# Kernel tuning notes

Hardware: AMD Instinct MI355X
Metric: run time of the kernel (lower is better)

Reference implementation:

```python
import jax, jax.numpy as jnp
import numpy as np
import math

B, S, D, H = 2, 1024, 4096, 32
HD = D // H  # 128
THETA = 500000.0


def setup_inputs() -> dict:
    key = jax.random.key(0)
    ks = jax.random.split(key, 6)
    x = jax.random.normal(ks[0], (B, S, D), dtype=jnp.float32)
    # RoPE frequencies (complex freqs_cis split into cos/sin), [S, HD//2]
    inv_freq = 1.0 / (THETA ** (jnp.arange(0, HD, 2, dtype=jnp.float32) / HD))
    angles = jnp.arange(S, dtype=jnp.float32)[:, None] * inv_freq[None, :]
    freqs_cos = jnp.cos(angles)
    freqs_sin = jnp.sin(angles)
    # Causal mask [1,1,S,S]: 0 on/below diag, large negative above
    neg = jnp.full((S, S), -1e9, dtype=jnp.float32)
    mask = jnp.triu(neg, k=1)[None, None]
    cache_k = jnp.zeros((B, S, H, HD), dtype=jnp.float32)
    cache_v = jnp.zeros((B, S, H, HD), dtype=jnp.float32)
    sc = 0.02
    wq = jax.random.normal(ks[1], (D, D), dtype=jnp.float32) * sc
    wk = jax.random.normal(ks[2], (D, D), dtype=jnp.float32) * sc
    wv = jax.random.normal(ks[3], (D, D), dtype=jnp.float32) * sc
    wo = jax.random.normal(ks[4], (D, D), dtype=jnp.float32) * sc
    return {"x": x, "freqs_cos": freqs_cos, "freqs_sin": freqs_sin,
            "mask": mask, "cache_k": cache_k, "cache_v": cache_v,
            "wq": wq, "wk": wk, "wv": wv, "wo": wo, "start_pos": 0}


def _apply_rope(t, cos, sin):
    # t: [B,S,H,HD]; cos/sin: [S,HD//2] -> complex multiply on (even, odd) pairs
    b, s, h, hd = t.shape
    tr = t.reshape(b, s, h, hd // 2, 2)
    te, to = tr[..., 0], tr[..., 1]
    c = cos[None, :, None, :]
    sn = sin[None, :, None, :]
    oe = te * c - to * sn
    oo = te * sn + to * c
    return jnp.stack([oe, oo], axis=-1).reshape(b, s, h, hd)


def reference(x, freqs_cos, freqs_sin, mask, cache_k, cache_v, wq, wk, wv, wo, start_pos):
    bsz, seqlen, dim = x.shape
    xq = (x @ wq.T).reshape(bsz, seqlen, H, HD)
    xk = (x @ wk.T).reshape(bsz, seqlen, H, HD)
    xv = (x @ wv.T).reshape(bsz, seqlen, H, HD)
    xq = _apply_rope(xq, freqs_cos, freqs_sin)
    xk = _apply_rope(xk, freqs_cos, freqs_sin)
    # KV-cache update
    cache_k = jax.lax.dynamic_update_slice(cache_k, xk, (0, start_pos, 0, 0))
    cache_v = jax.lax.dynamic_update_slice(cache_v, xv, (0, start_pos, 0, 0))
    keys = cache_k[:bsz, : start_pos + seqlen]    # [B,K,H,HD]
    values = cache_v[:bsz, : start_pos + seqlen]
    scores = jnp.einsum("bqhd,bkhd->bhqk", xq, keys) / math.sqrt(HD)
    scores = scores + mask
    probs = jax.nn.softmax(scores.astype(jnp.float32), axis=-1).astype(xq.dtype)
    out = jnp.einsum("bhqk,bkhd->bqhd", probs, values).reshape(bsz, seqlen, dim)
    return out @ wo.T
```

## Files before the change

### kernel.cpp

```cpp
#include <hip/hip_runtime.h>
#include <cstdint>
#include <cstddef>

typedef __bf16 bf16;
typedef bf16  bf16x8  __attribute__((ext_vector_type(8)));
typedef bf16  bf16x4  __attribute__((ext_vector_type(4)));
typedef float floatx4 __attribute__((ext_vector_type(4)));

#define D_MODEL 4096
#define NROWS   2048
#define SEQ     1024
#define NHEADS  32
#define HDIM    128

__device__ __forceinline__ void async16(const void* g, void* s) {
    __builtin_amdgcn_global_load_lds(
        (__attribute__((address_space(1))) void*)g,
        (__attribute__((address_space(3))) void*)s,
        16, 0, 0);
}

__global__ __launch_bounds__(256) void cvt_kernel(const float* __restrict__ in,
                                                  bf16* __restrict__ out, int n4) {
    int i = blockIdx.x * 256 + threadIdx.x;
    if (i >= n4) return;
    const float4 v = ((const float4*)in)[i];
    bf16x4 o;
    o[0] = (bf16)v.x; o[1] = (bf16)v.y; o[2] = (bf16)v.z; o[3] = (bf16)v.w;
    ((bf16x4*)out)[i] = o;
}

__global__ __launch_bounds__(256) void rope_kernel(bf16* __restrict__ Qb,
                                                   bf16* __restrict__ Kb,
                                                   const float* __restrict__ fc,
                                                   const float* __restrict__ fs) {
    int t = blockIdx.x * 256 + threadIdx.x;
    const bool isK = (t >> 20) != 0;
    bf16* p = isK ? Kb : Qb;
    const float qs = isK ? 1.0f : 0.08838834764831845f;
    int i = t & 1048575;
    int e = i * 8;
    int row = e >> 12;
    int coff = e & 4095;
    int s = row & 1023;
    int d0 = (coff & 127) >> 1;

    bf16x8 v = *(bf16x8*)(p + (size_t)row * D_MODEL + coff);
    float4 c4 = *(const float4*)&fc[s * 64 + d0];
    float4 s4 = *(const float4*)&fs[s * 64 + d0];
    float cc[4] = {c4.x, c4.y, c4.z, c4.w};
    float ss[4] = {s4.x, s4.y, s4.z, s4.w};
    bf16x8 o;
#pragma unroll
    for (int j = 0; j < 4; j++) {
        float e0 = (float)v[2 * j], e1 = (float)v[2 * j + 1];
        o[2 * j]     = (bf16)((e0 * cc[j] - e1 * ss[j]) * qs);
        o[2 * j + 1] = (bf16)((e0 * ss[j] + e1 * cc[j]) * qs);
    }
    *(bf16x8*)(p + (size_t)row * D_MODEL + coff) = o;
}

template<bool F32OUT>
__global__ __launch_bounds__(256) void gemm_bt(const bf16* __restrict__ A,
                                               const bf16* __restrict__ B0,
                                               void* __restrict__ C0) {
    __shared__ __align__(16) bf16 As[128 * 32];
    __shared__ __align__(16) bf16 Bs[128 * 32];
    const int tid  = threadIdx.x;
    const int lane = tid & 63;
    const int wave = tid >> 6;
    const int col  = lane & 15;
    const int quad = lane >> 4;
    const int bm = blockIdx.x * 128;
    const int bn = blockIdx.y * 128;
    const int wm = (wave >> 1) * 64;
    const int wn = (wave & 1) * 64;
    const bf16* Bw = B0 + (size_t)blockIdx.z * ((size_t)D_MODEL * D_MODEL);

    floatx4 acc[4][4] = {};

    for (int k0 = 0; k0 < D_MODEL; k0 += 32) {
#pragma unroll
        for (int j = 0; j < 2; j++) {
            int c   = j * 256 + tid;
            int row = c >> 2;
            int kc  = (c & 3) * 8;
            void* dstA = (void*)(As + (size_t)(j * 256 + wave * 64) * 8);
            void* dstB = (void*)(Bs + (size_t)(j * 256 + wave * 64) * 8);
            async16(A  + (size_t)(bm + row) * D_MODEL + k0 + kc, dstA);
            async16(Bw + (size_t)(bn + row) * D_MODEL + k0 + kc, dstB);
        }
        __syncthreads();
        bf16x8 a[4], b[4];
#pragma unroll
        for (int i = 0; i < 4; i++)
            a[i] = *(const bf16x8*)&As[(wm + i * 16 + col) * 32 + quad * 8];
#pragma unroll
        for (int j = 0; j < 4; j++)
            b[j] = *(const bf16x8*)&Bs[(wn + j * 16 + col) * 32 + quad * 8];
#pragma unroll
        for (int i = 0; i < 4; i++)
#pragma unroll
            for (int j = 0; j < 4; j++)
                acc[i][j] = __builtin_amdgcn_mfma_f32_16x16x32_bf16(a[i], b[j], acc[i][j], 0, 0, 0);
        __syncthreads();
    }

#pragma unroll
    for (int i = 0; i < 4; i++) {
#pragma unroll
        for (int j = 0; j < 4; j++) {
            int row = bm + wm + i * 16 + quad * 4;
            int cg  = bn + wn + j * 16 + col;
#pragma unroll
            for (int r = 0; r < 4; r++) {
                if constexpr (F32OUT) {
                    ((float*)C0)[(size_t)(row + r) * D_MODEL + cg] = acc[i][j][r];
                } else {
                    bf16* C = (bf16*)C0 + (size_t)blockIdx.z * ((size_t)NROWS * D_MODEL);
                    C[(size_t)(row + r) * D_MODEL + cg] = (bf16)acc[i][j][r];
                }
            }
        }
    }
}

#define PST 72

__global__ __launch_bounds__(256, 2) void attn_kernel(const bf16* __restrict__ Qb,
                                                      const bf16* __restrict__ Kb,
                                                      const bf16* __restrict__ Vb,
                                                      bf16* __restrict__ Ob) {
    __shared__ __align__(16) bf16 Ks[64 * 128];
    __shared__ __align__(16) bf16 Vt[128 * 64];
    __shared__ __align__(16) bf16 Ps[4 * 32 * PST];

    const int tid  = threadIdx.x;
    const int lane = tid & 63;
    const int wave = tid >> 6;
    const int col  = lane & 15;
    const int quad = lane >> 4;
    const int hb   = tid & 15;
    const int kb   = tid >> 4;

    const int b   = blockIdx.z;
    const int h   = blockIdx.y;
    const int ex  = b ? (7 - blockIdx.x) : blockIdx.x;
    const int q0b = ex * 128;
    const int q0w = q0b + wave * 32;
    const size_t bh = (size_t)(b * SEQ) * D_MODEL + h * HDIM;

    bf16x8 qf[2][4];
#pragma unroll
    for (int qi = 0; qi < 2; qi++)
#pragma unroll
        for (int kc = 0; kc < 4; kc++)
            qf[qi][kc] = *(const bf16x8*)(Qb + bh + (size_t)(q0w + qi * 16 + col) * D_MODEL + kc * 32 + quad * 8);

    floatx4 o[2][8];
    floatx4 ol[2];
#pragma unroll
    for (int qi = 0; qi < 2; qi++) {
        ol[qi] = (floatx4){0.f, 0.f, 0.f, 0.f};
#pragma unroll
        for (int c = 0; c < 8; c++) o[qi][c] = (floatx4){0.f, 0.f, 0.f, 0.f};
    }

    bf16x8 ones;
#pragma unroll
    for (int t = 0; t < 8; t++) ones[t] = (bf16)1.0f;

    bf16* Psw = Ps + wave * 32 * PST;
    const int nkt = ex * 2 + 2;

    for (int kt = 0; kt < nkt; kt++) {
        const int key0 = kt * 64;
#pragma unroll
        for (int it = 0; it < 4; it++) {
            int l = it * 256 + tid;
            int row = l >> 4, p = l & 15;
            int g = (p & 8) | ((p ^ (row & 7) ^ ((row >> 3) & 7)) & 7);
            async16(Kb + bh + (size_t)(key0 + row) * D_MODEL + g * 8,
                    (void*)(Ks + (size_t)(it * 256 + wave * 64) * 8));
        }
        {
            uint32_t uv[4][4];
#pragma unroll
            for (int i = 0; i < 4; i++) {
                uint4 t = *(const uint4*)(Vb + bh + (size_t)(key0 + kb * 4 + i) * D_MODEL + hb * 8);
                uv[i][0] = t.x; uv[i][1] = t.y; uv[i][2] = t.z; uv[i][3] = t.w;
            }
#pragma unroll
            for (int j = 0; j < 8; j++) {
                uint32_t sel = (j & 1) ? 0x07060302u : 0x05040100u;
                uint32_t w0 = __builtin_amdgcn_perm(uv[1][j >> 1], uv[0][j >> 1], sel);
                uint32_t w1 = __builtin_amdgcn_perm(uv[3][j >> 1], uv[2][j >> 1], sel);
                int row = hb * 8 + j;
                int p = ((kb >> 1) ^ (row & 7) ^ ((row >> 3) & 7)) & 7;
                uint2* dst = (uint2*)&Vt[row * 64 + p * 8 + (kb & 1) * 4];
                *dst = (uint2){w0, w1};
            }
        }
        __syncthreads();

        if (key0 <= q0w + 31) {
            const bool masked = (key0 + 63 > q0w);
            floatx4 sf[2][4];
#pragma unroll
            for (int qi = 0; qi < 2; qi++)
#pragma unroll
                for (int f = 0; f < 4; f++) sf[qi][f] = (floatx4){0.f, 0.f, 0.f, 0.f};
#pragma unroll
            for (int kc = 0; kc < 4; kc++)
#pragma unroll
                for (int f = 0; f < 4; f++) {
                    int row = f * 16 + col;
                    int g = kc * 4 + quad;
                    int p = (g & 8) | ((g ^ (row & 7) ^ ((row >> 3) & 7)) & 7);
                    bf16x8 kf = *(const bf16x8*)&Ks[row * 128 + p * 8];
                    sf[0][f] = __builtin_amdgcn_mfma_f32_16x16x32_bf16(qf[0][kc], kf, sf[0][f], 0, 0, 0);
                    sf[1][f] = __builtin_amdgcn_mfma_f32_16x16x32_bf16(qf[1][kc], kf, sf[1][f], 0, 0, 0);
                }
#pragma unroll
            for (int qi = 0; qi < 2; qi++)
#pragma unroll
                for (int f = 0; f < 4; f++) {
                    int key = key0 + f * 16 + col;
#pragma unroll
                    for (int r = 0; r < 4; r++) {
                        float pv;
                        if (masked)
                            pv = (key <= q0w + qi * 16 + quad * 4 + r) ? __expf(sf[qi][f][r]) : 0.f;
                        else
                            pv = __expf(sf[qi][f][r]);
                        Psw[(qi * 16 + quad * 4 + r) * PST + f * 16 + col] = (bf16)pv;
                    }
                }
#pragma unroll
            for (int kc = 0; kc < 2; kc++) {
                bf16x8 pa0 = *(const bf16x8*)&Psw[(0 * 16 + col) * PST + kc * 32 + quad * 8];
                bf16x8 pa1 = *(const bf16x8*)&Psw[(1 * 16 + col) * PST + kc * 32 + quad * 8];
                ol[0] = __builtin_amdgcn_mfma_f32_16x16x32_bf16(pa0, ones, ol[0], 0, 0, 0);
                ol[1] = __builtin_amdgcn_mfma_f32_16x16x32_bf16(pa1, ones, ol[1], 0, 0, 0);
#pragma unroll
                for (int c = 0; c < 8; c++) {
                    int row = c * 16 + col;
                    int g = kc * 4 + quad;
                    int p = (g ^ (row & 7) ^ ((row >> 3) & 7)) & 7;
                    bf16x8 vf = *(const bf16x8*)&Vt[row * 64 + p * 8];
                    o[0][c] = __builtin_amdgcn_mfma_f32_16x16x32_bf16(pa0, vf, o[0][c], 0, 0, 0);
                    o[1][c] = __builtin_amdgcn_mfma_f32_16x16x32_bf16(pa1, vf, o[1][c], 0, 0, 0);
                }
            }
        }
        __syncthreads();
    }

#pragma unroll
    for (int qi = 0; qi < 2; qi++) {
        float inv[4];
#pragma unroll
        for (int r = 0; r < 4; r++) inv[r] = 1.0f / ol[qi][r];
#pragma unroll
        for (int c = 0; c < 8; c++)
#pragma unroll
            for (int r = 0; r < 4; r++)
                Ob[bh + (size_t)(q0w + qi * 16 + quad * 4 + r) * D_MODEL + c * 16 + col] =
                    (bf16)(o[qi][c][r] * inv[r]);
    }
}

extern "C" void kernel_launch(void* const* d_in, const int* in_sizes, int n_in,
                              void* d_out, int out_size, void* d_ws, size_t ws_size,
                              hipStream_t stream) {
    const float* x  = (const float*)d_in[0];
    const float* fc = (const float*)d_in[1];
    const float* fs = (const float*)d_in[2];
    const float* wq = (const float*)d_in[6];
    const float* wk = (const float*)d_in[7];
    const float* wv = (const float*)d_in[8];
    const float* wo = (const float*)d_in[9];

    char* ws    = (char*)d_ws;
    bf16* xb    = (bf16*)(ws);
    bf16* wb    = (bf16*)(ws + 16777216ull);
    bf16* qkvb  = (bf16*)(ws + 117440512ull);
    bf16* attnb = (bf16*)(ws + 167772160ull);

    cvt_kernel<<<8192,  256, 0, stream>>>(x,  xb,                   2097152);
    cvt_kernel<<<16384, 256, 0, stream>>>(wq, wb + 0ull * 16777216, 4194304);
    cvt_kernel<<<16384, 256, 0, stream>>>(wk, wb + 1ull * 16777216, 4194304);
    cvt_kernel<<<16384, 256, 0, stream>>>(wv, wb + 2ull * 16777216, 4194304);

    gemm_bt<false><<<dim3(16, 32, 3), 256, 0, stream>>>(xb, wb, (void*)qkvb);

    cvt_kernel<<<16384, 256, 0, stream>>>(wo, wb, 4194304);

    rope_kernel<<<8192, 256, 0, stream>>>(qkvb, qkvb + 8388608ull, fc, fs);

    attn_kernel<<<dim3(8, 32, 2), 256, 0, stream>>>(qkvb, qkvb + 8388608ull,
                                                    qkvb + 16777216ull, attnb);

    gemm_bt<true><<<dim3(16, 32, 1), 256, 0, stream>>>(attnb, wb, d_out);
}
```

Before: 724.7 us.

## Fuse input conversions, retile attention to 64-row blocks, split-K output GEMM

Merges the x/wq/wk/wv fp32-to-bf16 conversions into one launch. Attention now assigns 16 query rows per wave (64 per block) with a blocked P layout in shared memory, doubling the block count for better load balance across the causal triangle. The output projection is split along K into two partial GEMMs followed by a reduction kernel, to raise parallelism. The extra fp32 partial buffers add memory traffic and an additional launch.

Result: slower. 739.2 us (+2.0%).

```diff
diff --git a/kernel.cpp b/kernel.cpp
--- a/kernel.cpp
+++ b/kernel.cpp
@@ -18,6 +18,30 @@
         (__attribute__((address_space(1))) void*)g,
         (__attribute__((address_space(3))) void*)s,
         16, 0, 0);
+}
+
+__global__ __launch_bounds__(256) void cvt4(const float* __restrict__ x,
+                                            const float* __restrict__ wq,
+                                            const float* __restrict__ wk,
+                                            const float* __restrict__ wv,
+                                            bf16* __restrict__ xb,
+                                            bf16* __restrict__ wb) {
+    int t = blockIdx.x * 256 + threadIdx.x;
+    const float* src;
+    bf16* dst;
+    int i;
+    if (t < 2097152) { src = x; dst = xb; i = t; }
+    else {
+        int j = t - 2097152;
+        int w = j >> 22;
+        i = j & 4194303;
+        src = (w == 0) ? wq : (w == 1) ? wk : wv;
+        dst = wb + (size_t)w * 16777216ull;
+    }
+    const float4 v = ((const float4*)src)[i];
+    bf16x4 o;
+    o[0] = (bf16)v.x; o[1] = (bf16)v.y; o[2] = (bf16)v.z; o[3] = (bf16)v.w;
+    ((bf16x4*)dst)[i] = o;
 }
 
 __global__ __launch_bounds__(256) void cvt_kernel(const float* __restrict__ in,
@@ -60,10 +84,9 @@
     *(bf16x8*)(p + (size_t)row * D_MODEL + coff) = o;
 }
 
-template<bool F32OUT>
-__global__ __launch_bounds__(256) void gemm_bt(const bf16* __restrict__ A,
-                                               const bf16* __restrict__ B0,
-                                               void* __restrict__ C0) {
+__global__ __launch_bounds__(256) void gemm_qkv(const bf16* __restrict__ A,
+                                                const bf16* __restrict__ B0,
+                                                bf16* __restrict__ C0) {
     __shared__ __align__(16) bf16 As[128 * 32];
     __shared__ __align__(16) bf16 Bs[128 * 32];
     const int tid  = threadIdx.x;
@@ -106,34 +129,94 @@
         __syncthreads();
     }
 
-#pragma unroll
-    for (int i = 0; i < 4; i++) {
+    bf16* C = C0 + (size_t)blockIdx.z * ((size_t)NROWS * D_MODEL);
+#pragma unroll
+    for (int i = 0; i < 4; i++)
 #pragma unroll
         for (int j = 0; j < 4; j++) {
             int row = bm + wm + i * 16 + quad * 4;
             int cg  = bn + wn + j * 16 + col;
 #pragma unroll
-            for (int r = 0; r < 4; r++) {
-                if constexpr (F32OUT) {
-                    ((float*)C0)[(size_t)(row + r) * D_MODEL + cg] = acc[i][j][r];
-                } else {
-                    bf16* C = (bf16*)C0 + (size_t)blockIdx.z * ((size_t)NROWS * D_MODEL);
-                    C[(size_t)(row + r) * D_MODEL + cg] = (bf16)acc[i][j][r];
-                }
-            }
-        }
-    }
-}
-
-#define PST 72
-
-__global__ __launch_bounds__(256, 2) void attn_kernel(const bf16* __restrict__ Qb,
-                                                      const bf16* __restrict__ Kb,
-                                                      const bf16* __restrict__ Vb,
-                                                      bf16* __restrict__ Ob) {
+            for (int r = 0; r < 4; r++)
+                C[(size_t)(row + r) * D_MODEL + cg] = (bf16)acc[i][j][r];
+        }
+}
+
+__global__ __launch_bounds__(256) void gemm_out(const bf16* __restrict__ A,
+                                                const bf16* __restrict__ B0,
+                                                float* __restrict__ part) {
+    __shared__ __align__(16) bf16 As[128 * 32];
+    __shared__ __align__(16) bf16 Bs[128 * 32];
+    const int tid  = threadIdx.x;
+    const int lane = tid & 63;
+    const int wave = tid >> 6;
+    const int col  = lane & 15;
+    const int quad = lane >> 4;
+    const int bm = blockIdx.x * 128;
+    const int bn = blockIdx.y * 128;
+    const int wm = (wave >> 1) * 64;
+    const int wn = (wave & 1) * 64;
+    const int kbase = blockIdx.z * 2048;
+
+    floatx4 acc[4][4] = {};
+
+    for (int k0 = kbase; k0 < kbase + 2048; k0 += 32) {
+#pragma unroll
+        for (int j = 0; j < 2; j++) {
+            int c   = j * 256 + tid;
+            int row = c >> 2;
+            int kc  = (c & 3) * 8;
+            void* dstA = (void*)(As + (size_t)(j * 256 + wave * 64) * 8);
+            void* dstB = (void*)(Bs + (size_t)(j * 256 + wave * 64) * 8);
+            async16(A  + (size_t)(bm + row) * D_MODEL + k0 + kc, dstA);
+            async16(B0 + (size_t)(bn + row) * D_MODEL + k0 + kc, dstB);
+        }
+        __syncthreads();
+        bf16x8 a[4], b[4];
+#pragma unroll
+        for (int i = 0; i < 4; i++)
+            a[i] = *(const bf16x8*)&As[(wm + i * 16 + col) * 32 + quad * 8];
+#pragma unroll
+        for (int j = 0; j < 4; j++)
+            b[j] = *(const bf16x8*)&Bs[(wn + j * 16 + col) * 32 + quad * 8];
+#pragma unroll
+        for (int i = 0; i < 4; i++)
+#pragma unroll
+            for (int j = 0; j < 4; j++)
+                acc[i][j] = __builtin_amdgcn_mfma_f32_16x16x32_bf16(a[i], b[j], acc[i][j], 0, 0, 0);
+        __syncthreads();
+    }
+
+    float* P = part + (size_t)blockIdx.z * ((size_t)NROWS * D_MODEL);
+#pragma unroll
+    for (int i = 0; i < 4; i++)
+#pragma unroll
+        for (int j = 0; j < 4; j++) {
+            int row = bm + wm + i * 16 + quad * 4;
+            int cg  = bn + wn + j * 16 + col;
+#pragma unroll
+            for (int r = 0; r < 4; r++)
+                P[(size_t)(row + r) * D_MODEL + cg] = acc[i][j][r];
+        }
+}
+
+__global__ __launch_bounds__(256) void reduce_kernel(const float* __restrict__ p0,
+                                                     const float* __restrict__ p1,
+                                                     float* __restrict__ out) {
+    int i = blockIdx.x * 256 + threadIdx.x;
+    float4 a = ((const float4*)p0)[i];
+    float4 b = ((const float4*)p1)[i];
+    float4 o = {a.x + b.x, a.y + b.y, a.z + b.z, a.w + b.w};
+    ((float4*)out)[i] = o;
+}
+
+__global__ __launch_bounds__(256) void attn_kernel(const bf16* __restrict__ Qb,
+                                                   const bf16* __restrict__ Kb,
+                                                   const bf16* __restrict__ Vb,
+                                                   bf16* __restrict__ Ob) {
     __shared__ __align__(16) bf16 Ks[64 * 128];
     __shared__ __align__(16) bf16 Vt[128 * 64];
-    __shared__ __align__(16) bf16 Ps[4 * 32 * PST];
+    __shared__ __align__(16) bf16 Ps[4 * 2048];
 
     const int tid  = threadIdx.x;
     const int lane = tid & 63;
@@ -143,35 +226,28 @@
     const int hb   = tid & 15;
     const int kb   = tid >> 4;
 
-    const int b   = blockIdx.z;
-    const int h   = blockIdx.y;
-    const int ex  = b ? (7 - blockIdx.x) : blockIdx.x;
-    const int q0b = ex * 128;
-    const int q0w = q0b + wave * 32;
-    const size_t bh = (size_t)(b * SEQ) * D_MODEL + h * HDIM;
-
-    bf16x8 qf[2][4];
-#pragma unroll
-    for (int qi = 0; qi < 2; qi++)
-#pragma unroll
-        for (int kc = 0; kc < 4; kc++)
-            qf[qi][kc] = *(const bf16x8*)(Qb + bh + (size_t)(q0w + qi * 16 + col) * D_MODEL + kc * 32 + quad * 8);
-
-    floatx4 o[2][8];
-    floatx4 ol[2];
-#pragma unroll
-    for (int qi = 0; qi < 2; qi++) {
-        ol[qi] = (floatx4){0.f, 0.f, 0.f, 0.f};
-#pragma unroll
-        for (int c = 0; c < 8; c++) o[qi][c] = (floatx4){0.f, 0.f, 0.f, 0.f};
-    }
+    const int batch = blockIdx.z;
+    const int h     = blockIdx.y;
+    const int ex    = batch ? (15 - blockIdx.x) : blockIdx.x;
+    const int q0w   = ex * 64 + wave * 16;
+    const size_t bh = (size_t)(batch * SEQ) * D_MODEL + h * HDIM;
+
+    bf16x8 qf[4];
+#pragma unroll
+    for (int kc = 0; kc < 4; kc++)
+        qf[kc] = *(const bf16x8*)(Qb + bh + (size_t)(q0w + col) * D_MODEL + kc * 32 + quad * 8);
+
+    floatx4 o[8];
+#pragma unroll
+    for (int c = 0; c < 8; c++) o[c] = (floatx4){0.f, 0.f, 0.f, 0.f};
+    floatx4 ol = (floatx4){0.f, 0.f, 0.f, 0.f};
 
     bf16x8 ones;
 #pragma unroll
     for (int t = 0; t < 8; t++) ones[t] = (bf16)1.0f;
 
-    bf16* Psw = Ps + wave * 32 * PST;
-    const int nkt = ex * 2 + 2;
+    bf16* Psw = Ps + wave * 2048;
+    const int nkt = ex + 1;
 
     for (int kt = 0; kt < nkt; kt++) {
         const int key0 = kt * 64;
@@ -203,71 +279,59 @@
         }
         __syncthreads();
 
-        if (key0 <= q0w + 31) {
-            const bool masked = (key0 + 63 > q0w);
-            floatx4 sf[2][4];
-#pragma unroll
-            for (int qi = 0; qi < 2; qi++)
-#pragma unroll
-                for (int f = 0; f < 4; f++) sf[qi][f] = (floatx4){0.f, 0.f, 0.f, 0.f};
-#pragma unroll
-            for (int kc = 0; kc < 4; kc++)
-#pragma unroll
-                for (int f = 0; f < 4; f++) {
-                    int row = f * 16 + col;
-                    int g = kc * 4 + quad;
-                    int p = (g & 8) | ((g ^ (row & 7) ^ ((row >> 3) & 7)) & 7);
-                    bf16x8 kf = *(const bf16x8*)&Ks[row * 128 + p * 8];
-                    sf[0][f] = __builtin_amdgcn_mfma_f32_16x16x32_bf16(qf[0][kc], kf, sf[0][f], 0, 0, 0);
-                    sf[1][f] = __builtin_amdgcn_mfma_f32_16x16x32_bf16(qf[1][kc], kf, sf[1][f], 0, 0, 0);
-                }
-#pragma unroll
-            for (int qi = 0; qi < 2; qi++)
-#pragma unroll
-                for (int f = 0; f < 4; f++) {
-                    int key = key0 + f * 16 + col;
-#pragma unroll
-                    for (int r = 0; r < 4; r++) {
-                        float pv;
-                        if (masked)
-                            pv = (key <= q0w + qi * 16 + quad * 4 + r) ? __expf(sf[qi][f][r]) : 0.f;
-                        else
-                            pv = __expf(sf[qi][f][r]);
-                        Psw[(qi * 16 + quad * 4 + r) * PST + f * 16 + col] = (bf16)pv;
-                    }
-                }
-#pragma unroll
-            for (int kc = 0; kc < 2; kc++) {
-                bf16x8 pa0 = *(const bf16x8*)&Psw[(0 * 16 + col) * PST + kc * 32 + quad * 8];
-                bf16x8 pa1 = *(const bf16x8*)&Psw[(1 * 16 + col) * PST + kc * 32 + quad * 8];
-                ol[0] = __builtin_amdgcn_mfma_f32_16x16x32_bf16(pa0, ones, ol[0], 0, 0, 0);
-                ol[1] = __builtin_amdgcn_mfma_f32_16x16x32_bf16(pa1, ones, ol[1], 0, 0, 0);
-#pragma unroll
-                for (int c = 0; c < 8; c++) {
-                    int row = c * 16 + col;
-                    int g = kc * 4 + quad;
-                    int p = (g ^ (row & 7) ^ ((row >> 3) & 7)) & 7;
-                    bf16x8 vf = *(const bf16x8*)&Vt[row * 64 + p * 8];
-                    o[0][c] = __builtin_amdgcn_mfma_f32_16x16x32_bf16(pa0, vf, o[0][c], 0, 0, 0);
-                    o[1][c] = __builtin_amdgcn_mfma_f32_16x16x32_bf16(pa1, vf, o[1][c], 0, 0, 0);
-                }
-            }
-        }
-        __syncthreads();
-    }
-
-#pragma unroll
-    for (int qi = 0; qi < 2; qi++) {
-        float inv[4];
-#pragma unroll
-        for (int r = 0; r < 4; r++) inv[r] = 1.0f / ol[qi][r];
-#pragma unroll
-        for (int c = 0; c < 8; c++)
-#pragma unroll
-            for (int r = 0; r < 4; r++)
-                Ob[bh + (size_t)(q0w + qi * 16 + quad * 4 + r) * D_MODEL + c * 16 + col] =
-                    (bf16)(o[qi][c][r] * inv[r]);
-    }
+        const bool masked = (kt == ex);
+        floatx4 sf[4];
+#pragma unroll
+        for (int f = 0; f < 4; f++) sf[f] = (floatx4){0.f, 0.f, 0.f, 0.f};
+#pragma unroll
+        for (int kc = 0; kc < 4; kc++)
+#pragma unroll
+            for (int f = 0; f < 4; f++) {
+                int row = f * 16 + col;
+                int g = kc * 4 + quad;
+                int p = (g & 8) | ((g ^ (row & 7) ^ ((row >> 3) & 7)) & 7);
+                bf16x8 kf = *(const bf16x8*)&Ks[row * 128 + p * 8];
+                sf[f] = __builtin_amdgcn_mfma_f32_16x16x32_bf16(qf[kc], kf, sf[f], 0, 0, 0);
+            }
+#pragma unroll
+        for (int f = 0; f < 4; f++) {
+            int key = key0 + f * 16 + col;
+            int fblk = (f >> 1) * 4 + (f & 1) * 2 + (col >> 3);
+#pragma unroll
+            for (int r = 0; r < 4; r++) {
+                float pv;
+                if (masked)
+                    pv = (key <= q0w + quad * 4 + r) ? __expf(sf[f][r]) : 0.f;
+                else
+                    pv = __expf(sf[f][r]);
+                Psw[fblk * 128 + (quad * 4 + r) * 8 + (col & 7)] = (bf16)pv;
+            }
+        }
+#pragma unroll
+        for (int kc = 0; kc < 2; kc++) {
+            bf16x8 pa = *(const bf16x8*)&Psw[((kc * 4 + quad) * 16 + col) * 8];
+            ol = __builtin_amdgcn_mfma_f32_16x16x32_bf16(pa, ones, ol, 0, 0, 0);
+#pragma unroll
+            for (int c = 0; c < 8; c++) {
+                int row = c * 16 + col;
+                int g = kc * 4 + quad;
+                int p = (g ^ (row & 7) ^ ((row >> 3) & 7)) & 7;
+                bf16x8 vf = *(const bf16x8*)&Vt[row * 64 + p * 8];
+                o[c] = __builtin_amdgcn_mfma_f32_16x16x32_bf16(pa, vf, o[c], 0, 0, 0);
+            }
+        }
+        __syncthreads();
+    }
+
+    float inv[4];
+#pragma unroll
+    for (int r = 0; r < 4; r++) inv[r] = 1.0f / ol[r];
+#pragma unroll
+    for (int c = 0; c < 8; c++)
+#pragma unroll
+        for (int r = 0; r < 4; r++)
+            Ob[bh + (size_t)(q0w + quad * 4 + r) * D_MODEL + c * 16 + col] =
+                (bf16)(o[c][r] * inv[r]);
 }
 
 extern "C" void kernel_launch(void* const* d_in, const int* in_sizes, int n_in,
@@ -281,25 +345,24 @@
     const float* wv = (const float*)d_in[8];
     const float* wo = (const float*)d_in[9];
 
-    char* ws    = (char*)d_ws;
-    bf16* xb    = (bf16*)(ws);
-    bf16* wb    = (bf16*)(ws + 16777216ull);
-    bf16* qkvb  = (bf16*)(ws + 117440512ull);
-    bf16* attnb = (bf16*)(ws + 167772160ull);
-
-    cvt_kernel<<<8192,  256, 0, stream>>>(x,  xb,                   2097152);
-    cvt_kernel<<<16384, 256, 0, stream>>>(wq, wb + 0ull * 16777216, 4194304);
-    cvt_kernel<<<16384, 256, 0, stream>>>(wk, wb + 1ull * 16777216, 4194304);
-    cvt_kernel<<<16384, 256, 0, stream>>>(wv, wb + 2ull * 16777216, 4194304);
-
-    gemm_bt<false><<<dim3(16, 32, 3), 256, 0, stream>>>(xb, wb, (void*)qkvb);
+    char*  ws    = (char*)d_ws;
+    bf16*  xb    = (bf16*)(ws);
+    bf16*  wb    = (bf16*)(ws + 16777216ull);
+    float* part  = (float*)(ws + 50331648ull);
+    bf16*  qkvb  = (bf16*)(ws + 117440512ull);
+    bf16*  attnb = (bf16*)(ws + 167772160ull);
+
+    cvt4<<<57344, 256, 0, stream>>>(x, wq, wk, wv, xb, wb);
+
+    gemm_qkv<<<dim3(16, 32, 3), 256, 0, stream>>>(xb, wb, qkvb);
 
     cvt_kernel<<<16384, 256, 0, stream>>>(wo, wb, 4194304);
 
     rope_kernel<<<8192, 256, 0, stream>>>(qkvb, qkvb + 8388608ull, fc, fs);
 
-    attn_kernel<<<dim3(8, 32, 2), 256, 0, stream>>>(qkvb, qkvb + 8388608ull,
-                                                    qkvb + 16777216ull, attnb);
-
-    gemm_bt<true><<<dim3(16, 32, 1), 256, 0, stream>>>(attnb, wb, d_out);
-}
+    attn_kernel<<<dim3(16, 32, 2), 256, 0, stream>>>(qkvb, qkvb + 8388608ull,
+                                                     qkvb + 16777216ull, attnb);
+
+    gemm_out<<<dim3(16, 32, 2), 256, 0, stream>>>(attnb, wb, part);
+    reduce_kernel<<<8192, 256, 0, stream>>>(part, part + 8388608ull, (float*)d_out);
+}
```
